# Kernel tuning notes

Measured on AMD Instinct MI355X. Metric: run time of the kernel, lower is better.

The kernel has to match this reference:

```python
import jax, jax.numpy as jnp
import numpy as np

B, L, H = 4, 1024, 1024          # docs, seq_len, hidden (LUKE-large)
NH, M, E, R = 16, 64, 24, 512    # attn heads, mentions/doc, entities/doc, pairs/doc
EMB, BLK, NCLS = 768, 64, 97     # embed_size, block_size, num_class


def setup_inputs() -> dict:
    key = jax.random.key(0)
    ks = jax.random.split(key, 10)
    s = 0.02
    return {
        "seq_lhs": jax.random.normal(ks[0], (B, L, H), jnp.float32),
        "ent_lhs": jax.random.normal(ks[1], (B, M, H), jnp.float32),
        "ent_to_seq_attn": jax.random.uniform(ks[2], (B, NH, M, L), jnp.float32),
        "entity_id_labels": jax.random.randint(ks[3], (B, M), 0, E),
        "hts": jax.random.randint(ks[4], (B, R, 2), 0, E),
        "Wh": jax.random.normal(ks[5], (2 * H, EMB), jnp.float32) * s,
        "bh": jnp.zeros((EMB,), jnp.float32),
        "Wt": jax.random.normal(ks[6], (2 * H, EMB), jnp.float32) * s,
        "bt": jnp.zeros((EMB,), jnp.float32),
        "Wb": jax.random.normal(ks[7], (EMB * BLK, 768), jnp.float32) * s,
        "bb": jnp.zeros((768,), jnp.float32),
        "Wc": jax.random.normal(ks[8], (768, NCLS), jnp.float32) * s,
        "bc": jnp.zeros((NCLS,), jnp.float32),
    }


def reference(seq_lhs, ent_lhs, ent_to_seq_attn, entity_id_labels, hts,
              Wh, bh, Wt, bt, Wb, bb, Wc, bc):
    dt = seq_lhs.dtype
    # mention -> entity segment mask [B, E, M]
    mask = entity_id_labels[:, None, :] == jnp.arange(E)[None, :, None]
    counts = mask.sum(-1)  # [B, E]
    # entity embedding: logsumexp over its mentions (== identity for 1 mention),
    # zeros for entities with no mentions
    masked = jnp.where(mask[..., None], ent_lhs[:, None, :, :], jnp.asarray(-1e30, dt))
    ent_emb = jax.scipy.special.logsumexp(masked, axis=2)           # [B, E, H]
    ent_emb = jnp.where((counts > 0)[..., None], ent_emb, jnp.asarray(0.0, dt))
    # entity -> seq attention: mean over mentions, zeros for empty entities
    mf = mask.astype(dt)
    ent_attn = jnp.einsum('bem,bhml->behl', mf, ent_to_seq_attn)    # [B, E, NH, L]
    ent_attn = ent_attn / jnp.maximum(counts, 1)[:, :, None, None].astype(dt)
    # gather per-pair head/tail embeddings and attentions
    h_idx, t_idx = hts[..., 0], hts[..., 1]                          # [B, R]
    hs = jnp.take_along_axis(ent_emb, h_idx[..., None], axis=1)      # [B, R, H]
    ts = jnp.take_along_axis(ent_emb, t_idx[..., None], axis=1)
    ha = jnp.take_along_axis(ent_attn, h_idx[..., None, None], axis=1)  # [B, R, NH, L]
    ta = jnp.take_along_axis(ent_attn, t_idx[..., None, None], axis=1)
    ht = (ha * ta).mean(2)                                           # [B, R, L]
    ht = ht / (ht.sum(-1, keepdims=True) + 1e-5)
    rel = jnp.einsum('bld,brl->brd', seq_lhs, ht)                    # [B, R, H]
    # head/tail extractors with context concat
    he = jnp.tanh(jnp.concatenate([hs, rel], -1) @ Wh + bh)          # [B, R, EMB]
    te = jnp.tanh(jnp.concatenate([ts, rel], -1) @ Wt + bt)
    K = EMB // BLK
    b1 = he.reshape(B * R, K, BLK)
    b2 = te.reshape(B * R, K, BLK)
    bl = (b1[:, :, :, None] * b2[:, :, None, :]).reshape(B * R, EMB * BLK)
    embeds = bl @ Wb + bb                                            # [B*R, 768]
    return embeds @ Wc + bc                                          # [B*R, NCLS]
```

## Files before the change

kernel.cpp:

```cpp
#include <hip/hip_runtime.h>
#include <stdint.h>
#include <math.h>

#define B_    4
#define L_    1024
#define H_    1024
#define NH_   16
#define M_    64
#define E_    24
#define R_    512
#define EMB_  768
#define BLK_  64
#define NCLS_ 97
#define NR_   2048
#define KBIG_ 49152
#define NCH_  768

typedef unsigned short ushort_t;
typedef unsigned int uint_t;
typedef short bf16x8 __attribute__((ext_vector_type(8)));
typedef float f32x4  __attribute__((ext_vector_type(4)));

__device__ __forceinline__ float bf2f(ushort_t u) {
    return __uint_as_float(((unsigned)u) << 16);
}
__device__ __forceinline__ ushort_t f2bf_rne(float f) {
    unsigned u = __float_as_uint(f);
    return (ushort_t)((u + 0x7fffu + ((u >> 16) & 1u)) >> 16);
}
__device__ __forceinline__ uint_t pack2_scale(uint_t tw, float h) {
    float lo = __uint_as_float(tw << 16) * h;
    float hi = __uint_as_float(tw & 0xffff0000u) * h;
    return __builtin_amdgcn_perm(__float_as_uint(hi), __float_as_uint(lo), 0x07060302u);
}

__global__ __launch_bounds__(256) void k_transpose_cvt(
    const float* __restrict__ in, ushort_t* __restrict__ out, int rows, int cols)
{
    __shared__ float t[64][65];
    int batch = blockIdx.z;
    in  += (size_t)batch * rows * cols;
    out += (size_t)batch * rows * cols;
    int c0 = blockIdx.x * 64, r0 = blockIdx.y * 64;
    int tx = threadIdx.x & 63, ty = threadIdx.x >> 6;
#pragma unroll
    for (int dr = 0; dr < 64; dr += 4)
        t[dr + ty][tx] = in[(size_t)(r0 + dr + ty) * cols + (c0 + tx)];
    __syncthreads();
    int c = threadIdx.x >> 2;
    int rk = (threadIdx.x & 3) * 16;
    ushort_t us[16];
#pragma unroll
    for (int q = 0; q < 16; q++) us[q] = f2bf_rne(t[rk + q][c]);
    ushort_t* op = &out[(size_t)(c0 + c) * rows + r0 + rk];
    *reinterpret_cast<int4*>(op)     = *reinterpret_cast<const int4*>(&us[0]);
    *reinterpret_cast<int4*>(op + 8) = *reinterpret_cast<const int4*>(&us[8]);
}

__global__ __launch_bounds__(256) void k_ent_emb(
    const float* __restrict__ ent_lhs, const int* __restrict__ labels,
    float* __restrict__ ent_emb)
{
    int b = blockIdx.x / E_, e = blockIdx.x % E_;
    __shared__ int list[M_];
    __shared__ int cnt;
    if (threadIdx.x == 0) cnt = 0;
    __syncthreads();
    if (threadIdx.x < M_ && labels[b * M_ + threadIdx.x] == e) {
        int p = atomicAdd(&cnt, 1);
        list[p] = threadIdx.x;
    }
    __syncthreads();
    int n = cnt;
    const float* base = ent_lhs + (size_t)b * M_ * H_;
    float* outp = ent_emb + ((size_t)b * E_ + e) * H_;
    for (int h = threadIdx.x; h < H_; h += blockDim.x) {
        if (n == 0) { outp[h] = 0.f; continue; }
        float mx = -1e30f;
        for (int i = 0; i < n; i++) mx = fmaxf(mx, base[(size_t)list[i] * H_ + h]);
        float s = 0.f;
        for (int i = 0; i < n; i++) s += __expf(base[(size_t)list[i] * H_ + h] - mx);
        outp[h] = mx + __logf(s);
    }
}

__global__ __launch_bounds__(256) void k_ent_attn(
    const float* __restrict__ attn, const int* __restrict__ labels,
    float* __restrict__ ent_attn)
{
    int idx = blockIdx.x;
    int nh = idx % NH_;
    int be = idx / NH_;
    int e = be % E_, b = be / E_;
    __shared__ int list[M_];
    __shared__ int cnt;
    if (threadIdx.x == 0) cnt = 0;
    __syncthreads();
    if (threadIdx.x < M_ && labels[b * M_ + threadIdx.x] == e) {
        int p = atomicAdd(&cnt, 1);
        list[p] = threadIdx.x;
    }
    __syncthreads();
    int n = cnt;
    float inv = 1.f / fmaxf((float)n, 1.f);
    const float* base = attn + ((size_t)b * NH_ + nh) * M_ * L_;
    float* outp = ent_attn + (((size_t)b * E_ + e) * NH_ + nh) * L_;
    for (int l = threadIdx.x; l < L_; l += blockDim.x) {
        float s = 0.f;
        for (int i = 0; i < n; i++) s += base[(size_t)list[i] * L_ + l];
        outp[l] = s * inv;
    }
}

__global__ __launch_bounds__(256) void k_ht(
    const float* __restrict__ ent_attn, const int* __restrict__ hts,
    ushort_t* __restrict__ ht_bf)
{
    int b = blockIdx.x / R_, r = blockIdx.x % R_;
    int h = hts[((size_t)b * R_ + r) * 2 + 0];
    int t = hts[((size_t)b * R_ + r) * 2 + 1];
    const float* ha = ent_attn + ((size_t)b * E_ + h) * NH_ * L_;
    const float* ta = ent_attn + ((size_t)b * E_ + t) * NH_ * L_;
    float vals[4];
    float local = 0.f;
#pragma unroll
    for (int p = 0; p < 4; p++) {
        int l = threadIdx.x + p * 256;
        float s = 0.f;
#pragma unroll
        for (int nh = 0; nh < NH_; nh++) s += ha[nh * L_ + l] * ta[nh * L_ + l];
        s *= (1.f / NH_);
        vals[p] = s;
        local += s;
    }
    __shared__ float red[4];
    float s = local;
#pragma unroll
    for (int off = 32; off > 0; off >>= 1) s += __shfl_down(s, off, 64);
    if ((threadIdx.x & 63) == 0) red[threadIdx.x >> 6] = s;
    __syncthreads();
    float tot = red[0] + red[1] + red[2] + red[3];
    float inv = 1.f / (tot + 1e-5f);
    ushort_t* outp = ht_bf + ((size_t)b * R_ + r) * L_;
#pragma unroll
    for (int p = 0; p < 4; p++) {
        int l = threadIdx.x + p * 256;
        outp[l] = f2bf_rne(vals[p] * inv);
    }
}

__global__ __launch_bounds__(256) void k_gather(
    const float* __restrict__ ent_emb, const int* __restrict__ hts,
    ushort_t* __restrict__ A1, ushort_t* __restrict__ A2)
{
    int n = blockIdx.x;
    int b = n / R_, r = n % R_;
    int h = hts[((size_t)b * R_ + r) * 2 + 0];
    int t = hts[((size_t)b * R_ + r) * 2 + 1];
    const float* eh = ent_emb + ((size_t)b * E_ + h) * H_;
    const float* et = ent_emb + ((size_t)b * E_ + t) * H_;
    for (int i = threadIdx.x; i < H_; i += 256) {
        A1[(size_t)n * 2048 + i] = f2bf_rne(eh[i]);
        A2[(size_t)n * 2048 + i] = f2bf_rne(et[i]);
    }
}

template <bool BIAS, bool TANH, bool DUAL>
__global__ __launch_bounds__(256) void k_gemm(
    const ushort_t* __restrict__ A, long sA, int lda,
    const ushort_t* __restrict__ Bt, long sB, int ldb,
    int K,
    const float* __restrict__ bias0, const float* __restrict__ bias1,
    ushort_t* __restrict__ C0, ushort_t* __restrict__ C1, long sC, int ldc)
{
    __shared__ ushort_t As[128 * 72];
    __shared__ ushort_t Bs[128 * 72];
    const int tid = threadIdx.x;
    const int lane = tid & 63, wid = tid >> 6;
    const int wr = wid >> 1, wc = wid & 1;
    const int z = blockIdx.z;
    const int m0 = blockIdx.y * 128, n0 = blockIdx.x * 128;
    A  += (long)z * sA;
    Bt += (long)z * sB;

    const f32x4 zero = {0.f, 0.f, 0.f, 0.f};
    f32x4 acc[4][4];
#pragma unroll
    for (int i = 0; i < 4; i++)
#pragma unroll
        for (int j = 0; j < 4; j++) acc[i][j] = zero;

    const int mrow = wr * 64 + (lane & 15);
    const int nrow = wc * 64 + (lane & 15);
    const int koff = (lane >> 4) * 8;

    for (int k0 = 0; k0 < K; k0 += 64) {
        __syncthreads();
#pragma unroll
        for (int p = 0; p < 4; p++) {
            int idx = tid + p * 256;
            int row = idx >> 3, seg = idx & 7;
            *reinterpret_cast<int4*>(&As[row * 72 + seg * 8]) =
                *reinterpret_cast<const int4*>(&A[(long)(m0 + row) * lda + k0 + seg * 8]);
            *reinterpret_cast<int4*>(&Bs[row * 72 + seg * 8]) =
                *reinterpret_cast<const int4*>(&Bt[(long)(n0 + row) * ldb + k0 + seg * 8]);
        }
        __syncthreads();
#pragma unroll
        for (int ks = 0; ks < 2; ks++) {
            bf16x8 af[4], bfg[4];
#pragma unroll
            for (int mt = 0; mt < 4; mt++)
                af[mt] = *reinterpret_cast<const bf16x8*>(&As[(mrow + mt * 16) * 72 + ks * 32 + koff]);
#pragma unroll
            for (int nt = 0; nt < 4; nt++)
                bfg[nt] = *reinterpret_cast<const bf16x8*>(&Bs[(nrow + nt * 16) * 72 + ks * 32 + koff]);
#pragma unroll
            for (int mt = 0; mt < 4; mt++)
#pragma unroll
                for (int nt = 0; nt < 4; nt++)
                    acc[mt][nt] = __builtin_amdgcn_mfma_f32_16x16x32_bf16(
                        af[mt], bfg[nt], acc[mt][nt], 0, 0, 0);
        }
    }

    const float* bias = BIAS ? (z ? bias1 : bias0) : nullptr;
#pragma unroll
    for (int mt = 0; mt < 4; mt++) {
#pragma unroll
        for (int nt = 0; nt < 4; nt++) {
#pragma unroll
            for (int rg = 0; rg < 4; rg++) {
                int row = m0 + wr * 64 + mt * 16 + (lane >> 4) * 4 + rg;
                int col = n0 + wc * 64 + nt * 16 + (lane & 15);
                float v = acc[mt][nt][rg];
                if (BIAS) v += bias[col];
                if (TANH) {
                    float vc = fminf(fmaxf(v, -15.f), 15.f);
                    float ex = __expf(2.f * vc);
                    v = (ex - 1.f) / (ex + 1.f);
                }
                ushort_t bv = f2bf_rne(v);
                C0[(long)z * sC + (long)row * ldc + col] = bv;
                if (DUAL) C1[(long)z * sC + (long)row * ldc + col] = bv;
            }
        }
    }
}

__global__ __launch_bounds__(256) void k_bilinear(
    const ushort_t* __restrict__ he, const ushort_t* __restrict__ te,
    const ushort_t* __restrict__ Wbt, float* __restrict__ embeds8, int splitz)
{
    __shared__ ushort_t TEs[128 * 72];
    __shared__ ushort_t HEs[128 * 72];
    const int tid = threadIdx.x;
    const int lane = tid & 63, wid = tid >> 6;
    const int wr = wid >> 1, wc = wid & 1;
    const int bid = blockIdx.x;
    const int z = bid & 7;
    const int w = bid >> 3;
    const int d0 = (w % 6) * 128, n0 = (w / 6) * 128;
    const int c0 = z * 96, cend = c0 + 96;

    const f32x4 zero = {0.f, 0.f, 0.f, 0.f};
    f32x4 acc[4][4];
#pragma unroll
    for (int i = 0; i < 4; i++)
#pragma unroll
        for (int j = 0; j < 4; j++) acc[i][j] = zero;

    const int mrow = wr * 64 + (lane & 15);
    const int drow = d0 + wc * 64 + (lane & 15);
    const int koff = (lane >> 4) * 8;

    int c = c0;
    while (c < cend) {
        const int k  = c >> 6;
        const int i0 = c & 63;
        const int i1 = min(64, i0 + (cend - c));
        __syncthreads();
#pragma unroll
        for (int p = 0; p < 4; p++) {
            int idx = tid + p * 256;
            int row = idx >> 3, seg = idx & 7;
            *reinterpret_cast<int4*>(&TEs[row * 72 + seg * 8]) =
                *reinterpret_cast<const int4*>(&te[(long)(n0 + row) * EMB_ + k * 64 + seg * 8]);
            *reinterpret_cast<int4*>(&HEs[row * 72 + seg * 8]) =
                *reinterpret_cast<const int4*>(&he[(long)(n0 + row) * EMB_ + k * 64 + seg * 8]);
        }
        __syncthreads();

        uint4 tef[4][2];
#pragma unroll
        for (int mt = 0; mt < 4; mt++)
#pragma unroll
            for (int ks = 0; ks < 2; ks++)
                tef[mt][ks] = *reinterpret_cast<const uint4*>(
                    &TEs[(mrow + mt * 16) * 72 + ks * 32 + koff]);

        for (int i = i0; i < i1; i++) {
            const long kkbase = (long)(k * 64 + i) * 64;
            bf16x8 bfr[4][2];
#pragma unroll
            for (int nt = 0; nt < 4; nt++)
#pragma unroll
                for (int ks = 0; ks < 2; ks++)
                    bfr[nt][ks] = *reinterpret_cast<const bf16x8*>(
                        &Wbt[(long)(drow + nt * 16) * KBIG_ + kkbase + ks * 32 + koff]);
            float hef[4];
#pragma unroll
            for (int mt = 0; mt < 4; mt++)
                hef[mt] = bf2f(HEs[(mrow + mt * 16) * 72 + i]);
#pragma unroll
            for (int mt = 0; mt < 4; mt++) {
#pragma unroll
                for (int ks = 0; ks < 2; ks++) {
                    uint4 t = tef[mt][ks];
                    union { uint_t u[4]; bf16x8 v; } a;
                    a.u[0] = pack2_scale(t.x, hef[mt]);
                    a.u[1] = pack2_scale(t.y, hef[mt]);
                    a.u[2] = pack2_scale(t.z, hef[mt]);
                    a.u[3] = pack2_scale(t.w, hef[mt]);
#pragma unroll
                    for (int nt = 0; nt < 4; nt++)
                        acc[mt][nt] = __builtin_amdgcn_mfma_f32_16x16x32_bf16(
                            a.v, bfr[nt][ks], acc[mt][nt], 0, 0, 0);
                }
            }
        }
        c += (i1 - i0);
    }

    float* outp = embeds8 + (splitz ? (long)z * NR_ * EMB_ : 0l);
#pragma unroll
    for (int mt = 0; mt < 4; mt++)
#pragma unroll
        for (int nt = 0; nt < 4; nt++)
#pragma unroll
            for (int rg = 0; rg < 4; rg++) {
                int n = n0 + wr * 64 + mt * 16 + (lane >> 4) * 4 + rg;
                int d = d0 + wc * 64 + nt * 16 + (lane & 15);
                if (splitz) outp[(long)n * EMB_ + d] = acc[mt][nt][rg];
                else        atomicAdd(&outp[(long)n * EMB_ + d], acc[mt][nt][rg]);
            }
}

__global__ __launch_bounds__(128) void k_final(
    const float* __restrict__ embeds8, int nz, const float* __restrict__ bb,
    const float* __restrict__ Wc, const float* __restrict__ bc,
    float* __restrict__ out)
{
    int n = blockIdx.x;
    __shared__ float row[EMB_];
    for (int i = threadIdx.x; i < EMB_; i += 128) {
        float s = bb[i];
        for (int zz = 0; zz < nz; zz++)
            s += embeds8[(size_t)zz * NR_ * EMB_ + (size_t)n * EMB_ + i];
        row[i] = s;
    }
    __syncthreads();
    int j = threadIdx.x;
    if (j < NCLS_) {
        float s = bc[j];
#pragma unroll 8
        for (int d = 0; d < EMB_; d++) s += row[d] * Wc[d * NCLS_ + j];
        out[(size_t)n * NCLS_ + j] = s;
    }
}

extern "C" void kernel_launch(void* const* d_in, const int* in_sizes, int n_in,
                              void* d_out, int out_size, void* d_ws, size_t ws_size,
                              hipStream_t stream)
{
    (void)in_sizes; (void)n_in; (void)out_size;
    const float* seq    = (const float*)d_in[0];
    const float* entl   = (const float*)d_in[1];
    const float* attn   = (const float*)d_in[2];
    const int*   labels = (const int*)d_in[3];
    const int*   hts    = (const int*)d_in[4];
    const float* Wh     = (const float*)d_in[5];
    const float* bh     = (const float*)d_in[6];
    const float* Wt     = (const float*)d_in[7];
    const float* bt     = (const float*)d_in[8];
    const float* Wb     = (const float*)d_in[9];
    const float* bb     = (const float*)d_in[10];
    const float* Wc     = (const float*)d_in[11];
    const float* bc     = (const float*)d_in[12];
    float* out = (float*)d_out;

    char* ws = (char*)d_ws;
    size_t off = 0;
    auto alloc = [&](size_t bytes) -> char* {
        char* p = ws + off;
        off += (bytes + 255) & ~(size_t)255;
        return p;
    };
    float*    ent_emb  = (float*)alloc((size_t)B_ * E_ * H_ * 4);
    float*    ent_attn = (float*)alloc((size_t)B_ * E_ * NH_ * L_ * 4);
    ushort_t* ht_bf    = (ushort_t*)alloc((size_t)B_ * R_ * L_ * 2);
    ushort_t* seq_t    = (ushort_t*)alloc((size_t)B_ * H_ * L_ * 2);
    ushort_t* A1       = (ushort_t*)alloc((size_t)NR_ * 2048 * 2);
    ushort_t* A2       = (ushort_t*)alloc((size_t)NR_ * 2048 * 2);
    ushort_t* Whb      = (ushort_t*)alloc((size_t)EMB_ * 2048 * 2);
    ushort_t* Wtb      = (ushort_t*)alloc((size_t)EMB_ * 2048 * 2);
    ushort_t* he_bf    = (ushort_t*)alloc((size_t)NR_ * EMB_ * 2);
    ushort_t* te_bf    = (ushort_t*)alloc((size_t)NR_ * EMB_ * 2);
    ushort_t* Wbt      = (ushort_t*)alloc((size_t)EMB_ * KBIG_ * 2);
    size_t embeds_off = off;
    int splitz = (ws_size >= embeds_off + (size_t)8 * NR_ * EMB_ * 4) ? 1 : 0;
    float* embeds8 = (float*)alloc((size_t)(splitz ? 8 : 1) * NR_ * EMB_ * 4);

    k_transpose_cvt<<<dim3(H_ / 64, L_ / 64, B_), 256, 0, stream>>>(seq, seq_t, L_, H_);
    k_transpose_cvt<<<dim3(EMB_ / 64, 2048 / 64, 1), 256, 0, stream>>>(Wh, Whb, 2048, EMB_);
    k_transpose_cvt<<<dim3(EMB_ / 64, 2048 / 64, 1), 256, 0, stream>>>(Wt, Wtb, 2048, EMB_);
    k_transpose_cvt<<<dim3(EMB_ / 64, KBIG_ / 64, 1), 256, 0, stream>>>(Wb, Wbt, KBIG_, EMB_);

    k_ent_emb<<<B_ * E_, 256, 0, stream>>>(entl, labels, ent_emb);
    k_ent_attn<<<B_ * E_ * NH_, 256, 0, stream>>>(attn, labels, ent_attn);

    k_ht<<<NR_, 256, 0, stream>>>(ent_attn, hts, ht_bf);
    k_gather<<<NR_, 256, 0, stream>>>(ent_emb, hts, A1, A2);

    k_gemm<false, false, true><<<dim3(H_ / 128, R_ / 128, B_), 256, 0, stream>>>(
        ht_bf, (long)R_ * L_, L_,
        seq_t, (long)H_ * L_, L_,
        L_, nullptr, nullptr,
        A1 + 1024, A2 + 1024, (long)R_ * 2048, 2048);

    k_gemm<true, true, false><<<dim3(EMB_ / 128, NR_ / 128, 2), 256, 0, stream>>>(
        A1, (long)NR_ * 2048, 2048,
        Whb, (long)EMB_ * 2048, 2048,
        2048, bh, bt,
        he_bf, nullptr, (long)NR_ * EMB_, EMB_);

    if (!splitz)
        (void)hipMemsetAsync(embeds8, 0, (size_t)NR_ * EMB_ * 4, stream);
    k_bilinear<<<768, 256, 0, stream>>>(he_bf, te_bf, Wbt, embeds8, splitz);

    k_final<<<NR_, 128, 0, stream>>>(embeds8, splitz ? 8 : 1, bb, Wc, bc, out);
}
```

Baseline: 727.4 us.

## Retile bilinear kernel with 16-way K split, register-prefetched weights, staged GEMM stores

The bilinear kernel now splits the 49152-long reduction 16 ways instead of 8, launching 1536 blocks. Each wave covers 32 rows by 128 output columns, up from 64 by 64, so every weight fragment feeds more MFMAs. Weight fragments for the next step are loaded into registers ahead of use with double buffering, and te is read from global memory instead of LDS. The generic GEMM epilogue now stages bf16 results in shared memory and writes them out as coalesced 16-byte stores. In exchange, the kernel uses more registers, needs 16 partial-sum slices of workspace, and k_final must do a longer reduction over those slices.

```diff
diff --git a/kernel.cpp b/kernel.cpp
--- a/kernel.cpp
+++ b/kernel.cpp
@@ -14,7 +14,6 @@
 #define NCLS_ 97
 #define NR_   2048
 #define KBIG_ 49152
-#define NCH_  768
 
 typedef unsigned short ushort_t;
 typedef unsigned int uint_t;
@@ -173,8 +172,9 @@
     const float* __restrict__ bias0, const float* __restrict__ bias1,
     ushort_t* __restrict__ C0, ushort_t* __restrict__ C1, long sC, int ldc)
 {
-    __shared__ ushort_t As[128 * 72];
-    __shared__ ushort_t Bs[128 * 72];
+    __shared__ ushort_t smem[2 * 128 * 72];
+    ushort_t* As = smem;
+    ushort_t* Bs = smem + 128 * 72;
     const int tid = threadIdx.x;
     const int lane = tid & 63, wid = tid >> 6;
     const int wr = wid >> 1, wc = wid & 1;
@@ -225,129 +225,153 @@
     }
 
     const float* bias = BIAS ? (z ? bias1 : bias0) : nullptr;
+    __syncthreads();
 #pragma unroll
     for (int mt = 0; mt < 4; mt++) {
 #pragma unroll
         for (int nt = 0; nt < 4; nt++) {
 #pragma unroll
             for (int rg = 0; rg < 4; rg++) {
-                int row = m0 + wr * 64 + mt * 16 + (lane >> 4) * 4 + rg;
-                int col = n0 + wc * 64 + nt * 16 + (lane & 15);
+                int row = wr * 64 + mt * 16 + (lane >> 4) * 4 + rg;
+                int col = wc * 64 + nt * 16 + (lane & 15);
                 float v = acc[mt][nt][rg];
-                if (BIAS) v += bias[col];
+                if (BIAS) v += bias[n0 + col];
                 if (TANH) {
                     float vc = fminf(fmaxf(v, -15.f), 15.f);
                     float ex = __expf(2.f * vc);
                     v = (ex - 1.f) / (ex + 1.f);
                 }
-                ushort_t bv = f2bf_rne(v);
-                C0[(long)z * sC + (long)row * ldc + col] = bv;
-                if (DUAL) C1[(long)z * sC + (long)row * ldc + col] = bv;
+                smem[row * 132 + col] = f2bf_rne(v);
             }
+        }
+    }
+    __syncthreads();
+    {
+        int row = tid >> 1, half = tid & 1;
+        const ushort_t* src = &smem[row * 132 + half * 64];
+        ushort_t* dst0 = &C0[(long)z * sC + (long)(m0 + row) * ldc + n0 + half * 64];
+#pragma unroll
+        for (int q = 0; q < 8; q++)
+            *reinterpret_cast<int4*>(dst0 + q * 8) = *reinterpret_cast<const int4*>(src + q * 8);
+        if (DUAL) {
+            ushort_t* dst1 = &C1[(long)z * sC + (long)(m0 + row) * ldc + n0 + half * 64];
+#pragma unroll
+            for (int q = 0; q < 8; q++)
+                *reinterpret_cast<int4*>(dst1 + q * 8) = *reinterpret_cast<const int4*>(src + q * 8);
         }
     }
 }
 
 __global__ __launch_bounds__(256) void k_bilinear(
     const ushort_t* __restrict__ he, const ushort_t* __restrict__ te,
-    const ushort_t* __restrict__ Wbt, float* __restrict__ embeds8, int splitz)
-{
-    __shared__ ushort_t TEs[128 * 72];
+    const ushort_t* __restrict__ Wbt, float* __restrict__ embedsN, int slices)
+{
     __shared__ ushort_t HEs[128 * 72];
     const int tid = threadIdx.x;
-    const int lane = tid & 63, wid = tid >> 6;
-    const int wr = wid >> 1, wc = wid & 1;
+    const int lane = tid & 63;
+    const int wr = tid >> 6;
     const int bid = blockIdx.x;
-    const int z = bid & 7;
-    const int w = bid >> 3;
+    const int z = ((bid & 7) << 1) | ((bid >> 3) & 1);
+    const int w = bid >> 4;
     const int d0 = (w % 6) * 128, n0 = (w / 6) * 128;
-    const int c0 = z * 96, cend = c0 + 96;
+    const int c0 = z * 48, cend = c0 + 48;
 
     const f32x4 zero = {0.f, 0.f, 0.f, 0.f};
-    f32x4 acc[4][4];
-#pragma unroll
-    for (int i = 0; i < 4; i++)
-#pragma unroll
-        for (int j = 0; j < 4; j++) acc[i][j] = zero;
-
-    const int mrow = wr * 64 + (lane & 15);
-    const int drow = d0 + wc * 64 + (lane & 15);
+    f32x4 acc[2][8];
+#pragma unroll
+    for (int i = 0; i < 2; i++)
+#pragma unroll
+        for (int j = 0; j < 8; j++) acc[i][j] = zero;
+
+    const int r15 = lane & 15;
+    const int mrow = wr * 32 + r15;
     const int koff = (lane >> 4) * 8;
 
     int c = c0;
     while (c < cend) {
-        const int k  = c >> 6;
+        const int kk = c >> 6;
         const int i0 = c & 63;
         const int i1 = min(64, i0 + (cend - c));
+
         __syncthreads();
 #pragma unroll
         for (int p = 0; p < 4; p++) {
             int idx = tid + p * 256;
             int row = idx >> 3, seg = idx & 7;
-            *reinterpret_cast<int4*>(&TEs[row * 72 + seg * 8]) =
-                *reinterpret_cast<const int4*>(&te[(long)(n0 + row) * EMB_ + k * 64 + seg * 8]);
             *reinterpret_cast<int4*>(&HEs[row * 72 + seg * 8]) =
-                *reinterpret_cast<const int4*>(&he[(long)(n0 + row) * EMB_ + k * 64 + seg * 8]);
+                *reinterpret_cast<const int4*>(&he[(long)(n0 + row) * EMB_ + kk * 64 + seg * 8]);
         }
         __syncthreads();
 
-        uint4 tef[4][2];
-#pragma unroll
-        for (int mt = 0; mt < 4; mt++)
+        uint4 tef[2][2];
+#pragma unroll
+        for (int mt = 0; mt < 2; mt++)
 #pragma unroll
             for (int ks = 0; ks < 2; ks++)
                 tef[mt][ks] = *reinterpret_cast<const uint4*>(
-                    &TEs[(mrow + mt * 16) * 72 + ks * 32 + koff]);
-
-        for (int i = i0; i < i1; i++) {
-            const long kkbase = (long)(k * 64 + i) * 64;
-            bf16x8 bfr[4][2];
-#pragma unroll
-            for (int nt = 0; nt < 4; nt++)
-#pragma unroll
-                for (int ks = 0; ks < 2; ks++)
-                    bfr[nt][ks] = *reinterpret_cast<const bf16x8*>(
-                        &Wbt[(long)(drow + nt * 16) * KBIG_ + kkbase + ks * 32 + koff]);
-            float hef[4];
-#pragma unroll
-            for (int mt = 0; mt < 4; mt++)
-                hef[mt] = bf2f(HEs[(mrow + mt * 16) * 72 + i]);
-#pragma unroll
-            for (int mt = 0; mt < 4; mt++) {
+                    &te[(long)(n0 + mrow + mt * 16) * EMB_ + kk * 64 + ks * 32 + koff]);
+
+        int4 b0[8][2], b1[8][2];
+        auto load_bfr = [&](int4 (&b)[8][2], int i) {
+            const long kb = (long)(kk * 64 + i) * 64 + koff;
+#pragma unroll
+            for (int nt = 0; nt < 8; nt++) {
+                const ushort_t* p = &Wbt[(long)(d0 + nt * 16 + r15) * KBIG_ + kb];
+                b[nt][0] = *reinterpret_cast<const int4*>(p);
+                b[nt][1] = *reinterpret_cast<const int4*>(p + 32);
+            }
+        };
+        auto compute = [&](int4 (&b)[8][2], int i) {
+#pragma unroll
+            for (int mt = 0; mt < 2; mt++) {
+                float h = bf2f(HEs[(mrow + mt * 16) * 72 + i]);
 #pragma unroll
                 for (int ks = 0; ks < 2; ks++) {
                     uint4 t = tef[mt][ks];
                     union { uint_t u[4]; bf16x8 v; } a;
-                    a.u[0] = pack2_scale(t.x, hef[mt]);
-                    a.u[1] = pack2_scale(t.y, hef[mt]);
-                    a.u[2] = pack2_scale(t.z, hef[mt]);
-                    a.u[3] = pack2_scale(t.w, hef[mt]);
-#pragma unroll
-                    for (int nt = 0; nt < 4; nt++)
+                    a.u[0] = pack2_scale(t.x, h);
+                    a.u[1] = pack2_scale(t.y, h);
+                    a.u[2] = pack2_scale(t.z, h);
+                    a.u[3] = pack2_scale(t.w, h);
+#pragma unroll
+                    for (int nt = 0; nt < 8; nt++)
                         acc[mt][nt] = __builtin_amdgcn_mfma_f32_16x16x32_bf16(
-                            a.v, bfr[nt][ks], acc[mt][nt], 0, 0, 0);
+                            a.v, *reinterpret_cast<const bf16x8*>(&b[nt][ks]), acc[mt][nt], 0, 0, 0);
                 }
             }
-        }
+        };
+
+        load_bfr(b0, i0);
+        int i = i0;
+        while (i + 2 <= i1) {
+            load_bfr(b1, i + 1);
+            compute(b0, i);
+            load_bfr(b0, (i + 2 < i1) ? i + 2 : i + 1);
+            compute(b1, i + 1);
+            i += 2;
+        }
+        if (i < i1) compute(b0, i);
         c += (i1 - i0);
     }
 
-    float* outp = embeds8 + (splitz ? (long)z * NR_ * EMB_ : 0l);
-#pragma unroll
-    for (int mt = 0; mt < 4; mt++)
-#pragma unroll
-        for (int nt = 0; nt < 4; nt++)
+    const int sl = (z * slices) >> 4;
+    float* outp = embedsN + (long)sl * NR_ * EMB_;
+    const bool plain = (slices == 16);
+#pragma unroll
+    for (int mt = 0; mt < 2; mt++)
+#pragma unroll
+        for (int nt = 0; nt < 8; nt++)
 #pragma unroll
             for (int rg = 0; rg < 4; rg++) {
-                int n = n0 + wr * 64 + mt * 16 + (lane >> 4) * 4 + rg;
-                int d = d0 + wc * 64 + nt * 16 + (lane & 15);
-                if (splitz) outp[(long)n * EMB_ + d] = acc[mt][nt][rg];
-                else        atomicAdd(&outp[(long)n * EMB_ + d], acc[mt][nt][rg]);
+                int n = n0 + wr * 32 + mt * 16 + (lane >> 4) * 4 + rg;
+                int d = d0 + nt * 16 + r15;
+                if (plain) outp[(long)n * EMB_ + d] = acc[mt][nt][rg];
+                else       atomicAdd(&outp[(long)n * EMB_ + d], acc[mt][nt][rg]);
             }
 }
 
 __global__ __launch_bounds__(128) void k_final(
-    const float* __restrict__ embeds8, int nz, const float* __restrict__ bb,
+    const float* __restrict__ embedsN, int nz, const float* __restrict__ bb,
     const float* __restrict__ Wc, const float* __restrict__ bc,
     float* __restrict__ out)
 {
@@ -356,7 +380,7 @@
     for (int i = threadIdx.x; i < EMB_; i += 128) {
         float s = bb[i];
         for (int zz = 0; zz < nz; zz++)
-            s += embeds8[(size_t)zz * NR_ * EMB_ + (size_t)n * EMB_ + i];
+            s += embedsN[(size_t)zz * NR_ * EMB_ + (size_t)n * EMB_ + i];
         row[i] = s;
     }
     __syncthreads();
@@ -407,9 +431,11 @@
     ushort_t* he_bf    = (ushort_t*)alloc((size_t)NR_ * EMB_ * 2);
     ushort_t* te_bf    = (ushort_t*)alloc((size_t)NR_ * EMB_ * 2);
     ushort_t* Wbt      = (ushort_t*)alloc((size_t)EMB_ * KBIG_ * 2);
-    size_t embeds_off = off;
-    int splitz = (ws_size >= embeds_off + (size_t)8 * NR_ * EMB_ * 4) ? 1 : 0;
-    float* embeds8 = (float*)alloc((size_t)(splitz ? 8 : 1) * NR_ * EMB_ * 4);
+
+    const size_t slice_b = (size_t)NR_ * EMB_ * 4;
+    int slices = (ws_size >= off + 16 * slice_b) ? 16
+               : (ws_size >= off + 8 * slice_b)  ? 8 : 1;
+    float* embedsN = (float*)alloc((size_t)slices * slice_b);
 
     k_transpose_cvt<<<dim3(H_ / 64, L_ / 64, B_), 256, 0, stream>>>(seq, seq_t, L_, H_);
     k_transpose_cvt<<<dim3(EMB_ / 64, 2048 / 64, 1), 256, 0, stream>>>(Wh, Whb, 2048, EMB_);
@@ -434,9 +460,9 @@
         2048, bh, bt,
         he_bf, nullptr, (long)NR_ * EMB_, EMB_);
 
-    if (!splitz)
-        (void)hipMemsetAsync(embeds8, 0, (size_t)NR_ * EMB_ * 4, stream);
-    k_bilinear<<<768, 256, 0, stream>>>(he_bf, te_bf, Wbt, embeds8, splitz);
-
-    k_final<<<NR_, 128, 0, stream>>>(embeds8, splitz ? 8 : 1, bb, Wc, bc, out);
-}
+    if (slices < 16)
+        (void)hipMemsetAsync(embedsN, 0, (size_t)slices * slice_b, stream);
+    k_bilinear<<<1536, 256, 0, stream>>>(he_bf, te_bf, Wbt, embedsN, slices);
+
+    k_final<<<NR_, 128, 0, stream>>>(embedsN, slices, bb, Wc, bc, out);
+}
```

New measurement: 1.017 ms. 39.7% more time.
